# Performance work log

Hardware: AMD Instinct MI355X
Metric: run time of the kernel (lower is better)

## Reference

```python
import jax, jax.numpy as jnp
import numpy as np

DIM = 512; QS = 64; QT = 16; KS = 256; KT = 16; WIN = 4; B = 8; RANK = 32


def build_local_mask():
    # centers = round(linspace(0, kv_steps-1, q_steps)); valid kv step iff |s - center| <= window
    centers = np.round(np.linspace(0.0, KS - 1, QS)).astype(np.int64)
    s = np.arange(KS)
    valid = np.abs(s[None, :] - centers[:, None]) <= WIN  # [QS, KS]
    m = np.where(valid, 0.0, -np.inf).astype(np.float32)
    m = np.repeat(np.repeat(m, QT, axis=0), KT, axis=1)  # [QS*QT, KS*KT]
    return jnp.asarray(m)


def layer_norm(x, g, b, eps=1e-5):
    mu = jnp.mean(x, axis=-1, keepdims=True)
    var = jnp.mean((x - mu) ** 2, axis=-1, keepdims=True)
    return (x - mu) * jax.lax.rsqrt(var + eps) * g + b


def setup_inputs() -> dict:
    key = jax.random.key(0)
    ks = jax.random.split(key, 16)
    w = lambda k, shape: (jax.random.normal(k, shape, jnp.float32) * 0.02)
    return {
        'query': jax.random.normal(ks[0], (B, QS, QT, DIM), jnp.float32),
        'source': jax.random.normal(ks[1], (B, KS, KT, DIM), jnp.float32),
        'ctx0': jax.random.normal(ks[2], (B, DIM), jnp.float32),
        'ctx1': jax.random.normal(ks[3], (B, DIM), jnp.float32),
        'mask': build_local_mask(),
        'qn_g': jnp.ones(DIM), 'qn_b': jnp.zeros(DIM),
        'kvn_g': jnp.ones(DIM), 'kvn_b': jnp.zeros(DIM),
        'Wq': w(ks[4], (DIM, DIM)), 'bq': jnp.zeros(DIM),
        'Wk': w(ks[5], (DIM, DIM)), 'bk': jnp.zeros(DIM),
        'Wv': w(ks[6], (DIM, DIM)), 'bv': jnp.zeros(DIM),
        'Wo': w(ks[7], (DIM, DIM)), 'bo': jnp.zeros(DIM),
        'Wgq': w(ks[8], (DIM, RANK)),
        'Wgk': w(ks[9], (DIM, RANK)),
        'Wc0': w(ks[10], (DIM, DIM)), 'bc0': jnp.zeros(DIM),
        'Wc1': w(ks[11], (DIM, DIM)), 'bc1': jnp.zeros(DIM),
        'Wf': w(ks[12], (DIM, 2 * DIM)), 'bf': jnp.zeros(2 * DIM),
    }


def reference(query, source, ctx0, ctx1, mask, qn_g, qn_b, kvn_g, kvn_b,
              Wq, bq, Wk, bk, Wv, bv, Wo, bo, Wgq, Wgk,
              Wc0, bc0, Wc1, bc1, Wf, bf):
    b = query.shape[0]
    # MultiContextCondition: per-context linear, pooled, FiLM head -> (gamma, beta)
    h = jax.nn.silu(ctx0 @ Wc0 + bc0 + ctx1 @ Wc1 + bc1)          # [b, dim]
    gamma, beta = jnp.split(h @ Wf + bf, 2, axis=-1)              # [b, dim] each
    q_flat = query.reshape(b, QS * QT, DIM)
    s_flat = source.reshape(b, KS * KT, DIM)
    q_base = layer_norm(q_flat, qn_g, qn_b)
    s_base = layer_norm(s_flat, kvn_g, kvn_b)
    q_mod = q_base * (1.0 + gamma[:, None, :]) + beta[:, None, :]
    q_p = q_mod @ Wq + bq
    k_p = s_base @ Wk + bk
    v_p = s_base @ Wv + bv
    scale = DIM ** -0.5
    scores = jnp.einsum('bqd,bkd->bqk', q_p, k_p) * scale          # [b, 1024, 4096]
    gate_q = q_p @ Wgq                                            # [b, q, rank]
    gate_k = k_p @ Wgk                                            # [b, k, rank]
    gate_logits = jnp.einsum('bqr,bkr->bqk', gate_q, gate_k) / np.float32(np.sqrt(RANK))
    gate_bias = jnp.log(jax.nn.sigmoid(gate_logits) + 1e-6)
    scores = scores + mask[None, :, :] + gate_bias
    attn = jax.nn.softmax(scores, axis=-1)
    out = jnp.einsum('bqk,bkd->bqd', attn, v_p) @ Wo + bo
    return out.reshape(b, QS, QT, DIM)
```

## Files before the change

kernel.cpp:

```cpp
#include <hip/hip_runtime.h>
#include <math.h>

#define DIMD 512
#define QS 64
#define KS 256
#define WIN 4
#define BATCH 8
#define RANK 32
#define NQ 1024
#define NK 4096
#define MQ (BATCH*NQ)
#define MK (BATCH*NK)

typedef unsigned short u16;
typedef __attribute__((ext_vector_type(8))) short bf16x8;
typedef __attribute__((ext_vector_type(4))) float f32x4;

__device__ inline u16 f2bf(float x) {
    union { float f; unsigned int u; } v; v.f = x;
    unsigned int r = v.u + 0x7FFF + ((v.u >> 16) & 1);
    return (u16)(r >> 16);
}
__device__ inline float bf2f(u16 x) {
    union { unsigned int u; float f; } v; v.u = ((unsigned int)x) << 16;
    return v.f;
}

__device__ __forceinline__ void gload16(const u16* g, u16* l) {
    __builtin_amdgcn_global_load_lds(
        (const __attribute__((address_space(1))) void*)g,
        (__attribute__((address_space(3))) void*)l, 16, 0, 0);
}


__device__ __forceinline__ void norm0_body(
    int bid, const float* __restrict__ X, const float* __restrict__ g,
    const float* __restrict__ bb, u16* __restrict__ out)
{
    int wave = threadIdx.x >> 6, lane = threadIdx.x & 63;
    long row = (long)bid * 4 + wave;
    const float* x = X + row * DIMD;
    int c = lane * 8;
    float4 a = *(const float4*)&x[c];
    float4 b = *(const float4*)&x[c + 4];
    float s  = a.x + a.y + a.z + a.w + b.x + b.y + b.z + b.w;
    float ss = a.x*a.x + a.y*a.y + a.z*a.z + a.w*a.w
             + b.x*b.x + b.y*b.y + b.z*b.z + b.w*b.w;
    #pragma unroll
    for (int o = 1; o < 64; o <<= 1) { s += __shfl_xor(s, o); ss += __shfl_xor(ss, o); }
    float mu = s * (1.f / DIMD);
    float var = ss * (1.f / DIMD) - mu * mu;
    float rs = rsqrtf(var + 1e-5f);
    float4 g0 = *(const float4*)&g[c],  g1 = *(const float4*)&g[c + 4];
    float4 b0 = *(const float4*)&bb[c], b1 = *(const float4*)&bb[c + 4];
    u16 o8[8];
    o8[0] = f2bf((a.x - mu) * rs * g0.x + b0.x);
    o8[1] = f2bf((a.y - mu) * rs * g0.y + b0.y);
    o8[2] = f2bf((a.z - mu) * rs * g0.z + b0.z);
    o8[3] = f2bf((a.w - mu) * rs * g0.w + b0.w);
    o8[4] = f2bf((b.x - mu) * rs * g1.x + b1.x);
    o8[5] = f2bf((b.y - mu) * rs * g1.y + b1.y);
    o8[6] = f2bf((b.z - mu) * rs * g1.z + b1.z);
    o8[7] = f2bf((b.w - mu) * rs * g1.w + b1.w);
    *(int4*)&out[row * DIMD + c] = *(const int4*)o8;
}

__device__ __forceinline__ void stats_body(
    int bid, const float* __restrict__ X, float* __restrict__ mu_o, float* __restrict__ rs_o)
{
    int wave = threadIdx.x >> 6, lane = threadIdx.x & 63;
    long row = (long)bid * 4 + wave;
    const float* x = X + row * DIMD;
    int c = lane * 8;
    float4 a = *(const float4*)&x[c];
    float4 b = *(const float4*)&x[c + 4];
    float s  = a.x + a.y + a.z + a.w + b.x + b.y + b.z + b.w;
    float ss = a.x*a.x + a.y*a.y + a.z*a.z + a.w*a.w
             + b.x*b.x + b.y*b.y + b.z*b.z + b.w*b.w;
    #pragma unroll
    for (int o = 1; o < 64; o <<= 1) { s += __shfl_xor(s, o); ss += __shfl_xor(ss, o); }
    if (lane == 0) {
        float mu = s * (1.f / DIMD);
        float var = ss * (1.f / DIMD) - mu * mu;
        mu_o[row] = mu;
        rs_o[row] = rsqrtf(var + 1e-5f);
    }
}

__device__ __forceinline__ void film_h_body(
    int bid, const float* __restrict__ ctx0, const float* __restrict__ ctx1,
    const float* __restrict__ Wc0, const float* __restrict__ bc0,
    const float* __restrict__ Wc1, const float* __restrict__ bc1,
    float* __restrict__ h)
{
    int b = bid >> 3;
    int d0 = (bid & 7) * 64;
    int t = threadIdx.x;
    int dl = t >> 2, p = t & 3;
    int d = d0 + dl;
    const float* c0 = ctx0 + b * DIMD;
    const float* c1 = ctx1 + b * DIMD;
    float acc = 0.f;
    #pragma unroll 4
    for (int ii = 0; ii < 128; ii++) {
        int i = p * 128 + ii;
        acc = fmaf(c0[i], Wc0[i * DIMD + d], acc);
        acc = fmaf(c1[i], Wc1[i * DIMD + d], acc);
    }
    acc += __shfl_xor(acc, 1);
    acc += __shfl_xor(acc, 2);
    if (p == 0) {
        float v = acc + bc0[d] + bc1[d];
        h[b * DIMD + d] = v / (1.f + expf(-v));
    }
}

__device__ __forceinline__ void film_gb_body(
    int bid, const float* __restrict__ h, const float* __restrict__ Wf,
    const float* __restrict__ bfv, float* __restrict__ gamma, float* __restrict__ beta)
{
    int b = bid >> 3;
    int d0 = (bid & 7) * 64;
    int t = threadIdx.x;
    int dl = t >> 2, p = t & 3;
    int d = d0 + dl;
    const float* hb = h + b * DIMD;
    float ga = 0.f, be = 0.f;
    #pragma unroll 4
    for (int ii = 0; ii < 128; ii++) {
        int i = p * 128 + ii;
        float hv = hb[i];
        ga = fmaf(hv, Wf[i * 2 * DIMD + d], ga);
        be = fmaf(hv, Wf[i * 2 * DIMD + DIMD + d], be);
    }
    ga += __shfl_xor(ga, 1); ga += __shfl_xor(ga, 2);
    be += __shfl_xor(be, 1); be += __shfl_xor(be, 2);
    if (p == 0) {
        gamma[b * DIMD + d] = ga + bfv[d];
        beta[b * DIMD + d]  = be + bfv[DIMD + d];
    }
}

__device__ __forceinline__ void transpose_body(
    int i, const float* __restrict__ src, u16* __restrict__ dst, int dst_row_off,
    float (*tile)[33])
{
    int t = threadIdx.x;
    int tx = t & 31, ty = t >> 5;
    int bx = (i & 15) * 32;
    int by = (i >> 4) * 32;
    #pragma unroll
    for (int k = 0; k < 4; k++)
        tile[ty + k * 8][tx] = src[(long)(by + ty + k * 8) * DIMD + bx + tx];
    __syncthreads();
    #pragma unroll
    for (int k = 0; k < 4; k++)
        dst[(long)(dst_row_off + bx + ty + k * 8) * DIMD + by + tx] = f2bf(tile[tx][ty + k * 8]);
}

__device__ __forceinline__ void gatefuse_body(
    int idx, const float* __restrict__ W, const float* __restrict__ Wg,
    u16* __restrict__ dst, int dst_row_off)
{
    int r = idx & 31, k = idx >> 5;
    float acc = 0.f;
    #pragma unroll 4
    for (int j = 0; j < DIMD; j++) acc = fmaf(W[k * DIMD + j], Wg[j * RANK + r], acc);
    dst[(long)(dst_row_off + r) * DIMD + k] = f2bf(acc);
}

__device__ __forceinline__ void biascat3_body(
    int bid, const float* __restrict__ b0, const float* __restrict__ b1,
    const float* __restrict__ Wg, float* __restrict__ dst)
{
    int t = bid * 256 + threadIdx.x;
    if (t < 512) dst[t] = b0[t];
    else if (t < 1024) dst[t] = b1[t - 512];
    else if (t < 1056) {
        int r = t - 1024;
        float a = 0.f;
        for (int j = 0; j < DIMD; j++) a = fmaf(b0[j], Wg[j * RANK + r], a);
        dst[t] = a;
    }
}

__device__ __forceinline__ void biascat2_body(
    int bid, const float* __restrict__ b0, const float* __restrict__ Wg,
    float* __restrict__ dst)
{
    int t = bid * 256 + threadIdx.x;
    if (t < 512) dst[t] = b0[t];
    else if (t < 544) {
        int r = t - 512;
        float a = 0.f;
        for (int j = 0; j < DIMD; j++) a = fmaf(b0[j], Wg[j * RANK + r], a);
        dst[t] = a;
    }
}

template<int NSEC, bool BF>
__device__ __forceinline__ void gemm_body(
    int id, const u16* __restrict__ A, const u16* __restrict__ Bt,
    const float* __restrict__ biascat,
    void* __restrict__ C0v, void* __restrict__ C1v, void* __restrict__ Cgv,
    int Nvalid, int nx, int ypg, u16* smem)
{
    u16* As = smem;
    u16* Bs = smem + 4096;

    int t = threadIdx.x;
    int wave = t >> 6, lane = t & 63;
    int xcd = id & 7, li = id >> 3;
    int by = xcd * ypg + li / nx;
    int bx = li % nx;
    int m0 = by * 128, n0 = bx * 128;
    int mhalf = (wave >> 1) * 64, nhalf = (wave & 1) * 64;
    int lm = lane & 15, quad = lane >> 4;

    int srow = wave * 32 + (lane >> 2);
    int scol = (lane & 3) * 8;
    const u16* Ag = A + (long)(m0 + srow) * DIMD + scol;
    const u16* Bg = Bt + (long)(n0 + srow) * DIMD + scol;
    u16* Asl = As + wave * 1024 + lane * 8;
    u16* Bsl = Bs + wave * 1024 + lane * 8;

    f32x4 acc[4][4];
    #pragma unroll
    for (int i = 0; i < 4; i++)
        #pragma unroll
        for (int j = 0; j < 4; j++)
            acc[i][j] = (f32x4){0.f, 0.f, 0.f, 0.f};

    for (int k0 = 0; k0 < DIMD; k0 += 32) {
        __syncthreads();
        gload16(Ag + k0, Asl);
        gload16(Ag + 16 * DIMD + k0, Asl + 512);
        gload16(Bg + k0, Bsl);
        gload16(Bg + 16 * DIMD + k0, Bsl + 512);
        __syncthreads();
        bf16x8 af[4], bfr[4];
        #pragma unroll
        for (int i = 0; i < 4; i++) {
            af[i]  = *(const bf16x8*)&As[(mhalf + i * 16 + lm) * 32 + quad * 8];
            bfr[i] = *(const bf16x8*)&Bs[(nhalf + i * 16 + lm) * 32 + quad * 8];
        }
        #pragma unroll
        for (int i = 0; i < 4; i++)
            #pragma unroll
            for (int j = 0; j < 4; j++)
                acc[i][j] = __builtin_amdgcn_mfma_f32_16x16x32_bf16(af[i], bfr[j], acc[i][j], 0, 0, 0);
    }

    float biasj[4];
    #pragma unroll
    for (int j = 0; j < 4; j++) biasj[j] = biascat[n0 + nhalf + j * 16 + lm];

    if (BF) {
        for (int i = 0; i < 4; i++) {
            __syncthreads();
            #pragma unroll
            for (int j = 0; j < 4; j++)
                #pragma unroll
                for (int r = 0; r < 4; r++)
                    smem[((wave >> 1) * 16 + quad * 4 + r) * 128 + nhalf + j * 16 + lm] =
                        f2bf(acc[i][j][r] + biasj[j]);
            __syncthreads();
            #pragma unroll
            for (int u = 0; u < 2; u++) {
                int cch = t + u * 256;
                int R = cch >> 4, ci = cch & 15;
                long grow = m0 + (R >> 4) * 64 + i * 16 + (R & 15);
                int gcol = n0 + ci * 8;
                int4 val = *(const int4*)&smem[R * 128 + ci * 8];
                if (NSEC == 1) {
                    *(int4*)((u16*)C0v + grow * 512 + gcol) = val;
                } else if (NSEC == 2) {
                    if (gcol < 512)          *(int4*)((u16*)C0v + grow * 512 + gcol) = val;
                    else if (gcol < Nvalid)  *(int4*)((u16*)Cgv + grow * 32 + (gcol - 512)) = val;
                } else {
                    if (gcol < 512)          *(int4*)((u16*)C0v + grow * 512 + gcol) = val;
                    else if (gcol < 1024)    *(int4*)((u16*)C1v + grow * 512 + (gcol - 512)) = val;
                    else if (gcol < Nvalid)  *(int4*)((u16*)Cgv + grow * 32 + (gcol - 1024)) = val;
                }
            }
        }
    } else {
        float* Stg = (float*)smem;
        for (int i = 0; i < 4; i++) {
            __syncthreads();
            #pragma unroll
            for (int j = 0; j < 4; j++)
                #pragma unroll
                for (int r = 0; r < 4; r++)
                    Stg[((wave >> 1) * 16 + quad * 4 + r) * 128 + nhalf + j * 16 + lm] =
                        acc[i][j][r] + biasj[j];
            __syncthreads();
            #pragma unroll
            for (int u = 0; u < 4; u++) {
                int cch = t + u * 256;
                int R = cch >> 5, ci = cch & 31;
                long grow = m0 + (R >> 4) * 64 + i * 16 + (R & 15);
                int gcol = n0 + ci * 4;
                *(float4*)((float*)C0v + grow * 512 + gcol) = *(const float4*)&Stg[R * 128 + ci * 4];
            }
        }
    }
}

#define PREP_NORM0   8192
#define PREP_STATS   (PREP_NORM0 + 2048)
#define PREP_TRANS   (PREP_STATS + 1024)
#define PREP_FILMH   (PREP_TRANS + 64)
#define PREP_GATE    (PREP_FILMH + 128)
#define PREP_TOTAL   (PREP_GATE + 8)

__global__ __launch_bounds__(256) void prep_kernel(
    const float* __restrict__ source, const float* __restrict__ kvn_g,
    const float* __restrict__ kvn_b, u16* __restrict__ sln,
    const float* __restrict__ query, float* __restrict__ mu_q, float* __restrict__ rs_q,
    const float* __restrict__ ctx0, const float* __restrict__ ctx1,
    const float* __restrict__ Wc0, const float* __restrict__ bc0,
    const float* __restrict__ Wc1, const float* __restrict__ bc1,
    float* __restrict__ h,
    const float* __restrict__ Wk, const float* __restrict__ Wv,
    const float* __restrict__ Wq, const float* __restrict__ Wo,
    u16* __restrict__ Btkv, u16* __restrict__ Btq, u16* __restrict__ Bto,
    const float* __restrict__ Wgk, const float* __restrict__ Wgq,
    const float* __restrict__ bk, const float* __restrict__ bv,
    const float* __restrict__ bq, float* __restrict__ biaskv,
    float* __restrict__ biasq)
{
    __shared__ float tile[32][33];
    int bid = blockIdx.x;
    if (bid < PREP_NORM0) {
        norm0_body(bid, source, kvn_g, kvn_b, sln);
    } else if (bid < PREP_STATS) {
        stats_body(bid - PREP_NORM0, query, mu_q, rs_q);
    } else if (bid < PREP_TRANS) {
        int tid = bid - PREP_STATS;
        int which = tid >> 8, i = tid & 255;
        if (which == 0)      transpose_body(i, Wk, Btkv, 0, tile);
        else if (which == 1) transpose_body(i, Wv, Btkv, 512, tile);
        else if (which == 2) transpose_body(i, Wq, Btq, 0, tile);
        else                 transpose_body(i, Wo, Bto, 0, tile);
    } else if (bid < PREP_FILMH) {
        film_h_body(bid - PREP_TRANS, ctx0, ctx1, Wc0, bc0, Wc1, bc1, h);
    } else if (bid < PREP_GATE) {
        int gid = bid - PREP_FILMH;
        int idx = (gid & 63) * 256 + threadIdx.x;
        if (gid < 64) gatefuse_body(idx, Wk, Wgk, Btkv, 1024);
        else          gatefuse_body(idx, Wq, Wgq, Btq, 512);
    } else {
        int cid = bid - PREP_GATE;
        if (cid < 5) biascat3_body(cid, bk, bv, Wgk, biaskv);
        else         biascat2_body(cid - 5, bq, Wgq, biasq);
    }
}

__global__ __launch_bounds__(256) void kv_kernel(
    const float* __restrict__ h, const float* __restrict__ Wf,
    const float* __restrict__ bfv, float* __restrict__ gamma, float* __restrict__ beta,
    const u16* __restrict__ sln, const u16* __restrict__ Btkv,
    const float* __restrict__ biaskv,
    u16* __restrict__ kp, u16* __restrict__ vp, u16* __restrict__ gk)
{
    __shared__ u16 smem[8192];
    int bid = blockIdx.x;
    if (bid < 64) {
        film_gb_body(bid, h, Wf, bfv, gamma, beta);
    } else {
        gemm_body<3, true>(bid - 64, sln, Btkv, biaskv, kp, vp, gk, 1056, 9, 32, smem);
    }
}

__global__ __launch_bounds__(256) void qproj_kernel(
    const float* __restrict__ query, const float* __restrict__ mu_q,
    const float* __restrict__ rs_q, const float* __restrict__ qn_g,
    const float* __restrict__ qn_b, const float* __restrict__ gamma,
    const float* __restrict__ beta, const u16* __restrict__ Btq,
    const float* __restrict__ biasq, u16* __restrict__ qp, u16* __restrict__ gq)
{
    __shared__ u16 smem[8192];
    u16* As = smem;
    u16* Bs = smem + 4096;

    int t = threadIdx.x;
    int wave = t >> 6, lane = t & 63;
    int id = blockIdx.x;
    int xcd = id & 7, li = id >> 3;
    int by = xcd * 8 + li / 5;
    int bx = li % 5;
    int m0 = by * 128, n0 = bx * 128;
    int mhalf = (wave >> 1) * 64, nhalf = (wave & 1) * 64;
    int lm = lane & 15, quad = lane >> 4;
    int bt = m0 >> 10;

    int srow = wave * 32 + (lane >> 2);
    int scol = (lane & 3) * 8;
    const u16* Bg = Btq + (long)(n0 + srow) * DIMD + scol;
    u16* Bsl = Bs + wave * 1024 + lane * 8;

    f32x4 acc[4][4];
    #pragma unroll
    for (int i = 0; i < 4; i++)
        #pragma unroll
        for (int j = 0; j < 4; j++)
            acc[i][j] = (f32x4){0.f, 0.f, 0.f, 0.f};

    for (int k0 = 0; k0 < DIMD; k0 += 32) {
        __syncthreads();
        gload16(Bg + k0, Bsl);
        gload16(Bg + 16 * DIMD + k0, Bsl + 512);
        #pragma unroll
        for (int u = 0; u < 2; u++) {
            int idx = t + u * 256;
            int r = idx >> 2;
            int c8 = (idx & 3) * 8;
            long grow = m0 + r;
            int col = k0 + c8;
            const float* xp = &query[grow * DIMD + col];
            float4 x0 = *(const float4*)xp, x1 = *(const float4*)(xp + 4);
            float mu = mu_q[grow], rs = rs_q[grow];
            float4 g0 = *(const float4*)&qn_g[col], g1 = *(const float4*)&qn_g[col + 4];
            float4 b0 = *(const float4*)&qn_b[col], b1 = *(const float4*)&qn_b[col + 4];
            const float* gp = gamma + bt * DIMD + col;
            const float* bp = beta + bt * DIMD + col;
            float4 gm0 = *(const float4*)gp, gm1 = *(const float4*)(gp + 4);
            float4 be0 = *(const float4*)bp, be1 = *(const float4*)(bp + 4);
            u16 o8[8];
            o8[0] = f2bf(((x0.x - mu) * rs * g0.x + b0.x) * (1.f + gm0.x) + be0.x);
            o8[1] = f2bf(((x0.y - mu) * rs * g0.y + b0.y) * (1.f + gm0.y) + be0.y);
            o8[2] = f2bf(((x0.z - mu) * rs * g0.z + b0.z) * (1.f + gm0.z) + be0.z);
            o8[3] = f2bf(((x0.w - mu) * rs * g0.w + b0.w) * (1.f + gm0.w) + be0.w);
            o8[4] = f2bf(((x1.x - mu) * rs * g1.x + b1.x) * (1.f + gm1.x) + be1.x);
            o8[5] = f2bf(((x1.y - mu) * rs * g1.y + b1.y) * (1.f + gm1.y) + be1.y);
            o8[6] = f2bf(((x1.z - mu) * rs * g1.z + b1.z) * (1.f + gm1.z) + be1.z);
            o8[7] = f2bf(((x1.w - mu) * rs * g1.w + b1.w) * (1.f + gm1.w) + be1.w);
            *(int4*)&As[r * 32 + c8] = *(const int4*)o8;
        }
        __syncthreads();
        bf16x8 af[4], bfr[4];
        #pragma unroll
        for (int i = 0; i < 4; i++) {
            af[i]  = *(const bf16x8*)&As[(mhalf + i * 16 + lm) * 32 + quad * 8];
            bfr[i] = *(const bf16x8*)&Bs[(nhalf + i * 16 + lm) * 32 + quad * 8];
        }
        #pragma unroll
        for (int i = 0; i < 4; i++)
            #pragma unroll
            for (int j = 0; j < 4; j++)
                acc[i][j] = __builtin_amdgcn_mfma_f32_16x16x32_bf16(af[i], bfr[j], acc[i][j], 0, 0, 0);
    }

    float biasj[4];
    #pragma unroll
    for (int j = 0; j < 4; j++) biasj[j] = biasq[n0 + nhalf + j * 16 + lm];

    for (int i = 0; i < 4; i++) {
        __syncthreads();
        #pragma unroll
        for (int j = 0; j < 4; j++)
            #pragma unroll
            for (int r = 0; r < 4; r++)
                smem[((wave >> 1) * 16 + quad * 4 + r) * 128 + nhalf + j * 16 + lm] =
                    f2bf(acc[i][j][r] + biasj[j]);
        __syncthreads();
        #pragma unroll
        for (int u = 0; u < 2; u++) {
            int cch = t + u * 256;
            int R = cch >> 4, ci = cch & 15;
            long grow = m0 + (R >> 4) * 64 + i * 16 + (R & 15);
            int gcol = n0 + ci * 8;
            int4 val = *(const int4*)&smem[R * 128 + ci * 8];
            if (gcol < 512)       *(int4*)(qp + grow * 512 + gcol) = val;
            else if (gcol < 544)  *(int4*)(gq + grow * 32 + (gcol - 512)) = val;
        }
    }
}

__global__ __launch_bounds__(256) void ogemm_kernel(
    const u16* __restrict__ ctxb, const u16* __restrict__ Bto,
    const float* __restrict__ bo, float* __restrict__ out)
{
    __shared__ u16 smem[8192];
    gemm_body<1, false>(blockIdx.x, ctxb, Bto, bo, out, nullptr, nullptr, 512, 4, 8, smem);
}

__global__ __launch_bounds__(256, 2) void attn_kernel(
    const u16* __restrict__ q_bf, const u16* __restrict__ k_bf,
    const u16* __restrict__ v_bf, const u16* __restrict__ gq_bf,
    const u16* __restrict__ gk_bf, u16* __restrict__ ctx)
{
    __shared__ u16 Ks[16 * 512];
    __shared__ u16 Vt[512 * 32];
    __shared__ u16 Pb[16 * 40];
    __shared__ float part[4][16][16];
    __shared__ float Gb[16][16];
    __shared__ float alphap[16];
    __shared__ float linv[16];

    int blk = blockIdx.x;
    int b = blk >> 6, qs = blk & 63;
    int center = (int)(qs * (255.0f / 63.0f) + 0.5f);
    int lo = center - WIN; if (lo < 0) lo = 0;
    int hi = center + WIN; if (hi > KS - 1) hi = KS - 1;
    int nst = hi - lo + 1;
    long rowq0 = (long)b * NQ + qs * 16;
    long rowk0 = (long)b * NK + lo * 16;

    int t = threadIdx.x;
    int wave = t >> 6, lane = t & 63;
    int lm = lane & 15, quad = lane >> 4;
    int qi = t >> 4, ki = t & 15;

    bf16x8 qf[4];
    #pragma unroll
    for (int f = 0; f < 4; f++)
        qf[f] = *(const bf16x8*)&q_bf[(rowq0 + lm) * DIMD + wave * 128 + f * 32 + quad * 8];
    bf16x8 gqf;
    if (wave == 3) gqf = *(const bf16x8*)&gq_bf[(rowq0 + lm) * RANK + quad * 8];

    int4 kpre[4], vpre[4];
    #pragma unroll
    for (int u = 0; u < 4; u++) {
        int idx = u * 256 + t;
        kpre[u] = *(const int4*)&k_bf[(rowk0 + (idx >> 6)) * DIMD + (idx & 63) * 8];
        int vkv = (idx >> 2) & 15, vdc = (idx & 3) | ((idx >> 6) << 2);
        vpre[u] = *(const int4*)&v_bf[(rowk0 + vkv) * DIMD + vdc * 8];
    }

    float m_run = -1e30f, l_run = 0.f;
    f32x4 acc[8];
    #pragma unroll
    for (int j = 0; j < 8; j++) acc[j] = (f32x4){0.f, 0.f, 0.f, 0.f};

    const float scale = 0.044194173824159216f;
    const float grs = 0.17677669529663687f;

    for (int s = 0; s < nst; s++) {
        int half = s & 1;
        #pragma unroll
        for (int u = 0; u < 4; u++) {
            int idx = u * 256 + t;
            int row = idx >> 6, c = idx & 63;
            *(int4*)&Ks[row * 512 + (c ^ (row & 7)) * 8] = kpre[u];
            int vkv = (idx >> 2) & 15, vdc = (idx & 3) | ((idx >> 6) << 2);
            int kvp = half * 16 + vkv;
            u16 vv[8];
            *(int4*)vv = vpre[u];
            #pragma unroll
            for (int i = 0; i < 8; i++) {
                int d = vdc * 8 + i;
                Vt[d * 32 + (((kvp >> 3) ^ (d & 3)) << 3) + (kvp & 7)] = vv[i];
            }
        }
        __syncthreads();
        if (s + 1 < nst) {
            long rk = rowk0 + (long)(s + 1) * 16;
            #pragma unroll
            for (int u = 0; u < 4; u++) {
                int idx = u * 256 + t;
                kpre[u] = *(const int4*)&k_bf[(rk + (idx >> 6)) * DIMD + (idx & 63) * 8];
                int vkv = (idx >> 2) & 15, vdc = (idx & 3) | ((idx >> 6) << 2);
                vpre[u] = *(const int4*)&v_bf[(rk + vkv) * DIMD + vdc * 8];
            }
        }
        f32x4 sacc = (f32x4){0.f, 0.f, 0.f, 0.f};
        #pragma unroll
        for (int f = 0; f < 4; f++) {
            int cidx = wave * 16 + f * 4 + quad;
            bf16x8 kf = *(const bf16x8*)&Ks[lm * 512 + (cidx ^ (lm & 7)) * 8];
            sacc = __builtin_amdgcn_mfma_f32_16x16x32_bf16(qf[f], kf, sacc, 0, 0, 0);
        }
        #pragma unroll
        for (int r = 0; r < 4; r++) part[wave][quad * 4 + r][lm] = sacc[r];
        if (wave == 3) {
            bf16x8 gkf = *(const bf16x8*)&gk_bf[(rowk0 + (long)s * 16 + lm) * RANK + quad * 8];
            f32x4 gacc = (f32x4){0.f, 0.f, 0.f, 0.f};
            gacc = __builtin_amdgcn_mfma_f32_16x16x32_bf16(gqf, gkf, gacc, 0, 0, 0);
            #pragma unroll
            for (int r = 0; r < 4; r++) Gb[quad * 4 + r][lm] = gacc[r];
        }
        __syncthreads();
        float sv = (part[0][qi][ki] + part[1][qi][ki] + part[2][qi][ki] + part[3][qi][ki]) * scale;
        float gl = Gb[qi][ki] * grs;
        float sig = 1.f / (1.f + expf(-gl));
        sv += logf(sig + 1e-6f);
        float mx = sv;
        mx = fmaxf(mx, __shfl_xor(mx, 1));
        mx = fmaxf(mx, __shfl_xor(mx, 2));
        mx = fmaxf(mx, __shfl_xor(mx, 4));
        mx = fmaxf(mx, __shfl_xor(mx, 8));
        float m_new = fmaxf(m_run, mx);
        float p = expf(sv - m_new);
        float ps = p;
        ps += __shfl_xor(ps, 1);
        ps += __shfl_xor(ps, 2);
        ps += __shfl_xor(ps, 4);
        ps += __shfl_xor(ps, 8);
        float alpha = expf(m_run - m_new);
        l_run = l_run * alpha + ps;
        m_run = m_new;
        Pb[qi * 40 + half * 16 + ki] = f2bf(p);
        if (half == 1) {
            Pb[qi * 40 + ki] = f2bf(bf2f(Pb[qi * 40 + ki]) * alpha);
        }
        bool dopv = (half == 1) || (s == nst - 1);
        if (dopv && half == 0) Pb[qi * 40 + 16 + ki] = 0;
        if (ki == 0) {
            if (half == 0) alphap[qi] = alpha;
            else           alphap[qi] *= alpha;
            if (s == nst - 1) linv[qi] = 1.f / l_run;
        }
        __syncthreads();
        if (dopv) {
            float ar[4];
            #pragma unroll
            for (int r = 0; r < 4; r++) ar[r] = alphap[quad * 4 + r];
            #pragma unroll
            for (int j = 0; j < 8; j++)
                #pragma unroll
                for (int r = 0; r < 4; r++) acc[j][r] *= ar[r];
            bf16x8 pf = *(const bf16x8*)&Pb[lm * 40 + quad * 8];
            #pragma unroll
            for (int j = 0; j < 8; j++) {
                int d = wave * 128 + j * 16 + lm;
                bf16x8 vf = *(const bf16x8*)&Vt[d * 32 + ((quad ^ (d & 3)) << 3)];
                acc[j] = __builtin_amdgcn_mfma_f32_16x16x32_bf16(pf, vf, acc[j], 0, 0, 0);
            }
            __syncthreads();
        }
    }
    float li[4];
    #pragma unroll
    for (int r = 0; r < 4; r++) li[r] = linv[quad * 4 + r];
    #pragma unroll
    for (int j = 0; j < 8; j++) {
        int d = wave * 128 + j * 16 + lm;
        #pragma unroll
        for (int r = 0; r < 4; r++)
            ctx[(rowq0 + quad * 4 + r) * DIMD + d] = f2bf(acc[j][r] * li[r]);
    }
}

extern "C" void kernel_launch(void* const* d_in, const int* in_sizes, int n_in,
                              void* d_out, int out_size, void* d_ws, size_t ws_size,
                              hipStream_t stream) {
    const float* query  = (const float*)d_in[0];
    const float* source = (const float*)d_in[1];
    const float* ctx0   = (const float*)d_in[2];
    const float* ctx1   = (const float*)d_in[3];
    const float* qn_g  = (const float*)d_in[5];
    const float* qn_b  = (const float*)d_in[6];
    const float* kvn_g = (const float*)d_in[7];
    const float* kvn_b = (const float*)d_in[8];
    const float* Wq = (const float*)d_in[9];   const float* bq = (const float*)d_in[10];
    const float* Wk = (const float*)d_in[11];  const float* bk = (const float*)d_in[12];
    const float* Wv = (const float*)d_in[13];  const float* bv = (const float*)d_in[14];
    const float* Wo = (const float*)d_in[15];  const float* bo = (const float*)d_in[16];
    const float* Wgq = (const float*)d_in[17];
    const float* Wgk = (const float*)d_in[18];
    const float* Wc0 = (const float*)d_in[19]; const float* bc0 = (const float*)d_in[20];
    const float* Wc1 = (const float*)d_in[21]; const float* bc1 = (const float*)d_in[22];
    const float* Wf  = (const float*)d_in[23]; const float* bfv = (const float*)d_in[24];

    float* ws = (float*)d_ws;
    float* h      = ws;
    float* gamma  = h + 4096;
    float* beta   = gamma + 4096;
    float* biaskv = beta + 4096;
    float* biasq  = biaskv + 1152;
    float* mu_q   = biasq + 640;
    float* rs_q   = mu_q + 8192;
    u16* u = (u16*)(rs_q + 8192);
    u16* sln  = u;                 u += (long)MK * DIMD;
    u16* kp   = u;                 u += (long)MK * DIMD;
    u16* vp   = u;                 u += (long)MK * DIMD;
    u16* gk   = u;                 u += (long)MK * RANK;
    u16* gq   = u;                 u += (long)MQ * RANK;
    u16* qp   = u;                 u += (long)MQ * DIMD;
    u16* ctxb = u;                 u += (long)MQ * DIMD;
    u16* Btkv = u;                 u += 1152L * DIMD;
    u16* Btq  = u;                 u += 640L * DIMD;
    u16* Bto  = u;                 u += 512L * DIMD;
    float* out = (float*)d_out;

    prep_kernel<<<PREP_TOTAL, 256, 0, stream>>>(
        source, kvn_g, kvn_b, sln,
        query, mu_q, rs_q,
        ctx0, ctx1, Wc0, bc0, Wc1, bc1, h,
        Wk, Wv, Wq, Wo, Btkv, Btq, Bto,
        Wgk, Wgq, bk, bv, bq, biaskv, biasq);

    kv_kernel<<<64 + 2304, 256, 0, stream>>>(
        h, Wf, bfv, gamma, beta, sln, Btkv, biaskv, kp, vp, gk);

    qproj_kernel<<<320, 256, 0, stream>>>(
        query, mu_q, rs_q, qn_g, qn_b, gamma, beta, Btq, biasq, qp, gq);

    attn_kernel<<<BATCH * QS, 256, 0, stream>>>(qp, kp, vp, gq, gk, ctxb);

    ogemm_kernel<<<256, 256, 0, stream>>>(ctxb, Bto, bo, out);
}
```

Measured before the change: 354.8 us.

## Fuse all stages into one persistent-dependency mega kernel with atomic flags

Replaces the five separate launches with a single kernel whose block ranges handle each stage. Inter-stage ordering now comes from per-tile atomic counters that consumer blocks spin on, so later stages can start as soon as their inputs are ready instead of waiting at kernel boundaries. It also merges the two FiLM steps into one block per batch, stages Wg in LDS for the gate-fused weights, and processes four rows per wave in the norm and stats stages. The scheme relies on blocks being dispatched in index order to avoid deadlock. Spin-waiting and the larger 64KB shared allocation may lower occupancy for the GEMM and attention stages.

```diff
diff --git a/kernel.cpp b/kernel.cpp
--- a/kernel.cpp
+++ b/kernel.cpp
@@ -32,117 +32,81 @@
         (__attribute__((address_space(3))) void*)l, 16, 0, 0);
 }
 
-
-__device__ __forceinline__ void norm0_body(
-    int bid, const float* __restrict__ X, const float* __restrict__ g,
-    const float* __restrict__ bb, u16* __restrict__ out)
-{
-    int wave = threadIdx.x >> 6, lane = threadIdx.x & 63;
-    long row = (long)bid * 4 + wave;
-    const float* x = X + row * DIMD;
-    int c = lane * 8;
-    float4 a = *(const float4*)&x[c];
-    float4 b = *(const float4*)&x[c + 4];
-    float s  = a.x + a.y + a.z + a.w + b.x + b.y + b.z + b.w;
-    float ss = a.x*a.x + a.y*a.y + a.z*a.z + a.w*a.w
-             + b.x*b.x + b.y*b.y + b.z*b.z + b.w*b.w;
-    #pragma unroll
-    for (int o = 1; o < 64; o <<= 1) { s += __shfl_xor(s, o); ss += __shfl_xor(ss, o); }
-    float mu = s * (1.f / DIMD);
-    float var = ss * (1.f / DIMD) - mu * mu;
-    float rs = rsqrtf(var + 1e-5f);
-    float4 g0 = *(const float4*)&g[c],  g1 = *(const float4*)&g[c + 4];
-    float4 b0 = *(const float4*)&bb[c], b1 = *(const float4*)&bb[c + 4];
-    u16 o8[8];
-    o8[0] = f2bf((a.x - mu) * rs * g0.x + b0.x);
-    o8[1] = f2bf((a.y - mu) * rs * g0.y + b0.y);
-    o8[2] = f2bf((a.z - mu) * rs * g0.z + b0.z);
-    o8[3] = f2bf((a.w - mu) * rs * g0.w + b0.w);
-    o8[4] = f2bf((b.x - mu) * rs * g1.x + b1.x);
-    o8[5] = f2bf((b.y - mu) * rs * g1.y + b1.y);
-    o8[6] = f2bf((b.z - mu) * rs * g1.z + b1.z);
-    o8[7] = f2bf((b.w - mu) * rs * g1.w + b1.w);
-    *(int4*)&out[row * DIMD + c] = *(const int4*)o8;
-}
-
-__device__ __forceinline__ void stats_body(
-    int bid, const float* __restrict__ X, float* __restrict__ mu_o, float* __restrict__ rs_o)
-{
-    int wave = threadIdx.x >> 6, lane = threadIdx.x & 63;
-    long row = (long)bid * 4 + wave;
-    const float* x = X + row * DIMD;
-    int c = lane * 8;
-    float4 a = *(const float4*)&x[c];
-    float4 b = *(const float4*)&x[c + 4];
-    float s  = a.x + a.y + a.z + a.w + b.x + b.y + b.z + b.w;
-    float ss = a.x*a.x + a.y*a.y + a.z*a.z + a.w*a.w
-             + b.x*b.x + b.y*b.y + b.z*b.z + b.w*b.w;
-    #pragma unroll
-    for (int o = 1; o < 64; o <<= 1) { s += __shfl_xor(s, o); ss += __shfl_xor(ss, o); }
-    if (lane == 0) {
-        float mu = s * (1.f / DIMD);
-        float var = ss * (1.f / DIMD) - mu * mu;
-        mu_o[row] = mu;
-        rs_o[row] = rsqrtf(var + 1e-5f);
-    }
-}
-
-__device__ __forceinline__ void film_h_body(
-    int bid, const float* __restrict__ ctx0, const float* __restrict__ ctx1,
+__device__ __forceinline__ void sigflag(int* f) {
+    __hip_atomic_fetch_add(f, 1, __ATOMIC_RELEASE, __HIP_MEMORY_SCOPE_AGENT);
+}
+__device__ __forceinline__ void waitflag(int* f, int target) {
+    if (threadIdx.x == 0) {
+        for (int i = 0; i < (1 << 22); i++) {
+            if (__hip_atomic_load(f, __ATOMIC_RELAXED, __HIP_MEMORY_SCOPE_AGENT) >= target)
+                break;
+            __builtin_amdgcn_s_sleep(8);
+        }
+    }
+    __syncthreads();
+}
+
+
+__device__ __forceinline__ void film_body(
+    int b, const float* __restrict__ ctx0, const float* __restrict__ ctx1,
     const float* __restrict__ Wc0, const float* __restrict__ bc0,
     const float* __restrict__ Wc1, const float* __restrict__ bc1,
-    float* __restrict__ h)
-{
-    int b = bid >> 3;
-    int d0 = (bid & 7) * 64;
+    const float* __restrict__ Wf, const float* __restrict__ bfv,
+    float* __restrict__ gamma, float* __restrict__ beta, float* hL)
+{
     int t = threadIdx.x;
-    int dl = t >> 2, p = t & 3;
-    int d = d0 + dl;
     const float* c0 = ctx0 + b * DIMD;
     const float* c1 = ctx1 + b * DIMD;
+    #pragma unroll
+    for (int half = 0; half < 2; half++) {
+        int d = t + half * 256;
+        float acc = bc0[d] + bc1[d];
+        #pragma unroll 4
+        for (int i = 0; i < DIMD; i++)
+            acc = fmaf(c0[i], Wc0[i * DIMD + d], fmaf(c1[i], Wc1[i * DIMD + d], acc));
+        hL[d] = acc / (1.f + expf(-acc));
+    }
+    __syncthreads();
+    #pragma unroll
+    for (int half = 0; half < 2; half++) {
+        int d = t + half * 256;
+        float ga = 0.f, be = 0.f;
+        #pragma unroll 4
+        for (int i = 0; i < DIMD; i++) {
+            float hv = hL[i];
+            ga = fmaf(hv, Wf[i * 2 * DIMD + d], ga);
+            be = fmaf(hv, Wf[i * 2 * DIMD + DIMD + d], be);
+        }
+        gamma[b * DIMD + d] = ga + bfv[d];
+        beta[b * DIMD + d]  = be + bfv[DIMD + d];
+    }
+}
+
+__device__ __forceinline__ void gatefuse_body(
+    int gid, const float* __restrict__ W, const float* __restrict__ Wg,
+    u16* __restrict__ dst, int off, float* WgL)
+{
+    int t = threadIdx.x;
+    for (int i = t; i < 4096; i += 256)
+        ((float4*)WgL)[i] = ((const float4*)Wg)[i];
+    __syncthreads();
+    int idx = gid * 256 + t;
+    int r = idx & 31, k = idx >> 5;
+    const float* Wr = W + (long)k * DIMD;
     float acc = 0.f;
     #pragma unroll 4
-    for (int ii = 0; ii < 128; ii++) {
-        int i = p * 128 + ii;
-        acc = fmaf(c0[i], Wc0[i * DIMD + d], acc);
-        acc = fmaf(c1[i], Wc1[i * DIMD + d], acc);
-    }
-    acc += __shfl_xor(acc, 1);
-    acc += __shfl_xor(acc, 2);
-    if (p == 0) {
-        float v = acc + bc0[d] + bc1[d];
-        h[b * DIMD + d] = v / (1.f + expf(-v));
-    }
-}
-
-__device__ __forceinline__ void film_gb_body(
-    int bid, const float* __restrict__ h, const float* __restrict__ Wf,
-    const float* __restrict__ bfv, float* __restrict__ gamma, float* __restrict__ beta)
-{
-    int b = bid >> 3;
-    int d0 = (bid & 7) * 64;
-    int t = threadIdx.x;
-    int dl = t >> 2, p = t & 3;
-    int d = d0 + dl;
-    const float* hb = h + b * DIMD;
-    float ga = 0.f, be = 0.f;
-    #pragma unroll 4
-    for (int ii = 0; ii < 128; ii++) {
-        int i = p * 128 + ii;
-        float hv = hb[i];
-        ga = fmaf(hv, Wf[i * 2 * DIMD + d], ga);
-        be = fmaf(hv, Wf[i * 2 * DIMD + DIMD + d], be);
-    }
-    ga += __shfl_xor(ga, 1); ga += __shfl_xor(ga, 2);
-    be += __shfl_xor(be, 1); be += __shfl_xor(be, 2);
-    if (p == 0) {
-        gamma[b * DIMD + d] = ga + bfv[d];
-        beta[b * DIMD + d]  = be + bfv[DIMD + d];
-    }
+    for (int j = 0; j < DIMD; j += 4) {
+        float4 w4 = *(const float4*)&Wr[j];
+        acc = fmaf(w4.x, WgL[(j + 0) * 32 + r], acc);
+        acc = fmaf(w4.y, WgL[(j + 1) * 32 + r], acc);
+        acc = fmaf(w4.z, WgL[(j + 2) * 32 + r], acc);
+        acc = fmaf(w4.w, WgL[(j + 3) * 32 + r], acc);
+    }
+    dst[(long)(off + r) * DIMD + k] = f2bf(acc);
 }
 
 __device__ __forceinline__ void transpose_body(
-    int i, const float* __restrict__ src, u16* __restrict__ dst, int dst_row_off,
+    int i, const float* __restrict__ src, u16* __restrict__ dst, int off,
     float (*tile)[33])
 {
     int t = threadIdx.x;
@@ -155,18 +119,7 @@
     __syncthreads();
     #pragma unroll
     for (int k = 0; k < 4; k++)
-        dst[(long)(dst_row_off + bx + ty + k * 8) * DIMD + by + tx] = f2bf(tile[tx][ty + k * 8]);
-}
-
-__device__ __forceinline__ void gatefuse_body(
-    int idx, const float* __restrict__ W, const float* __restrict__ Wg,
-    u16* __restrict__ dst, int dst_row_off)
-{
-    int r = idx & 31, k = idx >> 5;
-    float acc = 0.f;
-    #pragma unroll 4
-    for (int j = 0; j < DIMD; j++) acc = fmaf(W[k * DIMD + j], Wg[j * RANK + r], acc);
-    dst[(long)(dst_row_off + r) * DIMD + k] = f2bf(acc);
+        dst[(long)(off + bx + ty + k * 8) * DIMD + by + tx] = f2bf(tile[tx][ty + k * 8]);
 }
 
 __device__ __forceinline__ void biascat3_body(
@@ -183,7 +136,6 @@
         dst[t] = a;
     }
 }
-
 __device__ __forceinline__ void biascat2_body(
     int bid, const float* __restrict__ b0, const float* __restrict__ Wg,
     float* __restrict__ dst)
@@ -198,22 +150,79 @@
     }
 }
 
+__device__ __forceinline__ void norm0_body(
+    int bid, const float* __restrict__ X, const float* __restrict__ g,
+    const float* __restrict__ bb, u16* __restrict__ out)
+{
+    int wave = threadIdx.x >> 6, lane = threadIdx.x & 63;
+    int c = lane * 8;
+    float4 g0 = *(const float4*)&g[c],  g1 = *(const float4*)&g[c + 4];
+    float4 b0 = *(const float4*)&bb[c], b1 = *(const float4*)&bb[c + 4];
+    long row0 = (long)bid * 16 + wave * 4;
+    #pragma unroll
+    for (int rr = 0; rr < 4; rr++) {
+        long row = row0 + rr;
+        const float* x = X + row * DIMD;
+        float4 a = *(const float4*)&x[c];
+        float4 b = *(const float4*)&x[c + 4];
+        float s  = a.x + a.y + a.z + a.w + b.x + b.y + b.z + b.w;
+        float ss = a.x*a.x + a.y*a.y + a.z*a.z + a.w*a.w
+                 + b.x*b.x + b.y*b.y + b.z*b.z + b.w*b.w;
+        #pragma unroll
+        for (int o = 1; o < 64; o <<= 1) { s += __shfl_xor(s, o); ss += __shfl_xor(ss, o); }
+        float mu = s * (1.f / DIMD);
+        float var = ss * (1.f / DIMD) - mu * mu;
+        float rs = rsqrtf(var + 1e-5f);
+        u16 o8[8];
+        o8[0] = f2bf((a.x - mu) * rs * g0.x + b0.x);
+        o8[1] = f2bf((a.y - mu) * rs * g0.y + b0.y);
+        o8[2] = f2bf((a.z - mu) * rs * g0.z + b0.z);
+        o8[3] = f2bf((a.w - mu) * rs * g0.w + b0.w);
+        o8[4] = f2bf((b.x - mu) * rs * g1.x + b1.x);
+        o8[5] = f2bf((b.y - mu) * rs * g1.y + b1.y);
+        o8[6] = f2bf((b.z - mu) * rs * g1.z + b1.z);
+        o8[7] = f2bf((b.w - mu) * rs * g1.w + b1.w);
+        *(int4*)&out[row * DIMD + c] = *(const int4*)o8;
+    }
+}
+
+__device__ __forceinline__ void stats_body(
+    int bid, const float* __restrict__ X, float* __restrict__ mu_o, float* __restrict__ rs_o)
+{
+    int wave = threadIdx.x >> 6, lane = threadIdx.x & 63;
+    int c = lane * 8;
+    long row0 = (long)bid * 16 + wave * 4;
+    #pragma unroll
+    for (int rr = 0; rr < 4; rr++) {
+        long row = row0 + rr;
+        const float* x = X + row * DIMD;
+        float4 a = *(const float4*)&x[c];
+        float4 b = *(const float4*)&x[c + 4];
+        float s  = a.x + a.y + a.z + a.w + b.x + b.y + b.z + b.w;
+        float ss = a.x*a.x + a.y*a.y + a.z*a.z + a.w*a.w
+                 + b.x*b.x + b.y*b.y + b.z*b.z + b.w*b.w;
+        #pragma unroll
+        for (int o = 1; o < 64; o <<= 1) { s += __shfl_xor(s, o); ss += __shfl_xor(ss, o); }
+        if (lane == 0) {
+            float mu = s * (1.f / DIMD);
+            float var = ss * (1.f / DIMD) - mu * mu;
+            mu_o[row] = mu;
+            rs_o[row] = rsqrtf(var + 1e-5f);
+        }
+    }
+}
+
 template<int NSEC, bool BF>
 __device__ __forceinline__ void gemm_body(
-    int id, const u16* __restrict__ A, const u16* __restrict__ Bt,
+    int m0, int n0, const u16* __restrict__ A, const u16* __restrict__ Bt,
     const float* __restrict__ biascat,
     void* __restrict__ C0v, void* __restrict__ C1v, void* __restrict__ Cgv,
-    int Nvalid, int nx, int ypg, u16* smem)
+    int Nvalid, u16* smem)
 {
     u16* As = smem;
     u16* Bs = smem + 4096;
-
     int t = threadIdx.x;
     int wave = t >> 6, lane = t & 63;
-    int xcd = id & 7, li = id >> 3;
-    int by = xcd * ypg + li / nx;
-    int bx = li % nx;
-    int m0 = by * 128, n0 = bx * 128;
     int mhalf = (wave >> 1) * 64, nhalf = (wave & 1) * 64;
     int lm = lane & 15, quad = lane >> 4;
 
@@ -307,90 +316,18 @@
     }
 }
 
-#define PREP_NORM0   8192
-#define PREP_STATS   (PREP_NORM0 + 2048)
-#define PREP_TRANS   (PREP_STATS + 1024)
-#define PREP_FILMH   (PREP_TRANS + 64)
-#define PREP_GATE    (PREP_FILMH + 128)
-#define PREP_TOTAL   (PREP_GATE + 8)
-
-__global__ __launch_bounds__(256) void prep_kernel(
-    const float* __restrict__ source, const float* __restrict__ kvn_g,
-    const float* __restrict__ kvn_b, u16* __restrict__ sln,
-    const float* __restrict__ query, float* __restrict__ mu_q, float* __restrict__ rs_q,
-    const float* __restrict__ ctx0, const float* __restrict__ ctx1,
-    const float* __restrict__ Wc0, const float* __restrict__ bc0,
-    const float* __restrict__ Wc1, const float* __restrict__ bc1,
-    float* __restrict__ h,
-    const float* __restrict__ Wk, const float* __restrict__ Wv,
-    const float* __restrict__ Wq, const float* __restrict__ Wo,
-    u16* __restrict__ Btkv, u16* __restrict__ Btq, u16* __restrict__ Bto,
-    const float* __restrict__ Wgk, const float* __restrict__ Wgq,
-    const float* __restrict__ bk, const float* __restrict__ bv,
-    const float* __restrict__ bq, float* __restrict__ biaskv,
-    float* __restrict__ biasq)
-{
-    __shared__ float tile[32][33];
-    int bid = blockIdx.x;
-    if (bid < PREP_NORM0) {
-        norm0_body(bid, source, kvn_g, kvn_b, sln);
-    } else if (bid < PREP_STATS) {
-        stats_body(bid - PREP_NORM0, query, mu_q, rs_q);
-    } else if (bid < PREP_TRANS) {
-        int tid = bid - PREP_STATS;
-        int which = tid >> 8, i = tid & 255;
-        if (which == 0)      transpose_body(i, Wk, Btkv, 0, tile);
-        else if (which == 1) transpose_body(i, Wv, Btkv, 512, tile);
-        else if (which == 2) transpose_body(i, Wq, Btq, 0, tile);
-        else                 transpose_body(i, Wo, Bto, 0, tile);
-    } else if (bid < PREP_FILMH) {
-        film_h_body(bid - PREP_TRANS, ctx0, ctx1, Wc0, bc0, Wc1, bc1, h);
-    } else if (bid < PREP_GATE) {
-        int gid = bid - PREP_FILMH;
-        int idx = (gid & 63) * 256 + threadIdx.x;
-        if (gid < 64) gatefuse_body(idx, Wk, Wgk, Btkv, 1024);
-        else          gatefuse_body(idx, Wq, Wgq, Btq, 512);
-    } else {
-        int cid = bid - PREP_GATE;
-        if (cid < 5) biascat3_body(cid, bk, bv, Wgk, biaskv);
-        else         biascat2_body(cid - 5, bq, Wgq, biasq);
-    }
-}
-
-__global__ __launch_bounds__(256) void kv_kernel(
-    const float* __restrict__ h, const float* __restrict__ Wf,
-    const float* __restrict__ bfv, float* __restrict__ gamma, float* __restrict__ beta,
-    const u16* __restrict__ sln, const u16* __restrict__ Btkv,
-    const float* __restrict__ biaskv,
-    u16* __restrict__ kp, u16* __restrict__ vp, u16* __restrict__ gk)
-{
-    __shared__ u16 smem[8192];
-    int bid = blockIdx.x;
-    if (bid < 64) {
-        film_gb_body(bid, h, Wf, bfv, gamma, beta);
-    } else {
-        gemm_body<3, true>(bid - 64, sln, Btkv, biaskv, kp, vp, gk, 1056, 9, 32, smem);
-    }
-}
-
-__global__ __launch_bounds__(256) void qproj_kernel(
-    const float* __restrict__ query, const float* __restrict__ mu_q,
+__device__ __forceinline__ void qproj_body(
+    int m0, int n0, const float* __restrict__ query, const float* __restrict__ mu_q,
     const float* __restrict__ rs_q, const float* __restrict__ qn_g,
     const float* __restrict__ qn_b, const float* __restrict__ gamma,
     const float* __restrict__ beta, const u16* __restrict__ Btq,
-    const float* __restrict__ biasq, u16* __restrict__ qp, u16* __restrict__ gq)
-{
-    __shared__ u16 smem[8192];
+    const float* __restrict__ biasq, u16* __restrict__ qp, u16* __restrict__ gq,
+    u16* smem)
+{
     u16* As = smem;
     u16* Bs = smem + 4096;
-
     int t = threadIdx.x;
     int wave = t >> 6, lane = t & 63;
-    int id = blockIdx.x;
-    int xcd = id & 7, li = id >> 3;
-    int by = xcd * 8 + li / 5;
-    int bx = li % 5;
-    int m0 = by * 128, n0 = bx * 128;
     int mhalf = (wave >> 1) * 64, nhalf = (wave & 1) * 64;
     int lm = lane & 15, quad = lane >> 4;
     int bt = m0 >> 10;
@@ -478,28 +415,19 @@
     }
 }
 
-__global__ __launch_bounds__(256) void ogemm_kernel(
-    const u16* __restrict__ ctxb, const u16* __restrict__ Bto,
-    const float* __restrict__ bo, float* __restrict__ out)
-{
-    __shared__ u16 smem[8192];
-    gemm_body<1, false>(blockIdx.x, ctxb, Bto, bo, out, nullptr, nullptr, 512, 4, 8, smem);
-}
-
-__global__ __launch_bounds__(256, 2) void attn_kernel(
-    const u16* __restrict__ q_bf, const u16* __restrict__ k_bf,
+__device__ __forceinline__ void attn_body(
+    int blk, const u16* __restrict__ q_bf, const u16* __restrict__ k_bf,
     const u16* __restrict__ v_bf, const u16* __restrict__ gq_bf,
-    const u16* __restrict__ gk_bf, u16* __restrict__ ctx)
-{
-    __shared__ u16 Ks[16 * 512];
-    __shared__ u16 Vt[512 * 32];
-    __shared__ u16 Pb[16 * 40];
-    __shared__ float part[4][16][16];
-    __shared__ float Gb[16][16];
-    __shared__ float alphap[16];
-    __shared__ float linv[16];
-
-    int blk = blockIdx.x;
+    const u16* __restrict__ gk_bf, u16* __restrict__ ctx, char* SM)
+{
+    u16* Ks = (u16*)SM;
+    u16* Vt = (u16*)(SM + 16384);
+    u16* Pb = (u16*)(SM + 49152);
+    float* part = (float*)(SM + 50432);
+    float* Gb = (float*)(SM + 54528);
+    float* alphap = (float*)(SM + 55552);
+    float* linv = (float*)(SM + 55616);
+
     int b = blk >> 6, qs = blk & 63;
     int center = (int)(qs * (255.0f / 63.0f) + 0.5f);
     int lo = center - WIN; if (lo < 0) lo = 0;
@@ -573,17 +501,18 @@
             sacc = __builtin_amdgcn_mfma_f32_16x16x32_bf16(qf[f], kf, sacc, 0, 0, 0);
         }
         #pragma unroll
-        for (int r = 0; r < 4; r++) part[wave][quad * 4 + r][lm] = sacc[r];
+        for (int r = 0; r < 4; r++) part[wave * 256 + (quad * 4 + r) * 16 + lm] = sacc[r];
         if (wave == 3) {
             bf16x8 gkf = *(const bf16x8*)&gk_bf[(rowk0 + (long)s * 16 + lm) * RANK + quad * 8];
             f32x4 gacc = (f32x4){0.f, 0.f, 0.f, 0.f};
             gacc = __builtin_amdgcn_mfma_f32_16x16x32_bf16(gqf, gkf, gacc, 0, 0, 0);
             #pragma unroll
-            for (int r = 0; r < 4; r++) Gb[quad * 4 + r][lm] = gacc[r];
-        }
-        __syncthreads();
-        float sv = (part[0][qi][ki] + part[1][qi][ki] + part[2][qi][ki] + part[3][qi][ki]) * scale;
-        float gl = Gb[qi][ki] * grs;
+            for (int r = 0; r < 4; r++) Gb[(quad * 4 + r) * 16 + lm] = gacc[r];
+        }
+        __syncthreads();
+        float sv = (part[qi * 16 + ki] + part[256 + qi * 16 + ki]
+                  + part[512 + qi * 16 + ki] + part[768 + qi * 16 + ki]) * scale;
+        float gl = Gb[qi * 16 + ki] * grs;
         float sig = 1.f / (1.f + expf(-gl));
         sv += logf(sig + 1e-6f);
         float mx = sv;
@@ -643,6 +572,141 @@
     }
 }
 
+#define B_FILM  0
+#define B_GATE  8
+#define B_TRANS 136
+#define B_BIAS  1160
+#define B_STAT  1168
+#define B_NORM  1680
+#define B_KV    3728
+#define B_QP    6032
+#define B_ATTN  6352
+#define B_OG    6864
+#define B_TOTAL 7120
+
+__global__ __launch_bounds__(256, 2) void mega_kernel(
+    int* __restrict__ F,
+    const float* __restrict__ query, const float* __restrict__ source,
+    const float* __restrict__ ctx0, const float* __restrict__ ctx1,
+    const float* __restrict__ qn_g, const float* __restrict__ qn_b,
+    const float* __restrict__ kvn_g, const float* __restrict__ kvn_b,
+    const float* __restrict__ Wq, const float* __restrict__ bq,
+    const float* __restrict__ Wk, const float* __restrict__ bk,
+    const float* __restrict__ Wv, const float* __restrict__ bv,
+    const float* __restrict__ Wo, const float* __restrict__ bo,
+    const float* __restrict__ Wgq, const float* __restrict__ Wgk,
+    const float* __restrict__ Wc0, const float* __restrict__ bc0,
+    const float* __restrict__ Wc1, const float* __restrict__ bc1,
+    const float* __restrict__ Wf, const float* __restrict__ bfv,
+    float* __restrict__ gamma, float* __restrict__ beta,
+    float* __restrict__ biaskv, float* __restrict__ biasq,
+    float* __restrict__ mu_q, float* __restrict__ rs_q,
+    u16* __restrict__ sln, u16* __restrict__ kp, u16* __restrict__ vp,
+    u16* __restrict__ gk, u16* __restrict__ gq, u16* __restrict__ qp,
+    u16* __restrict__ ctxb, u16* __restrict__ Btkv, u16* __restrict__ Btq,
+    u16* __restrict__ Bto, float* __restrict__ out)
+{
+    __shared__ __align__(16) char SM[65536];
+    int* F_SLN = F;
+    int* F_QST = F + 256;
+    int* F_FILM = F + 320;
+    int* F_WKV = F + 321;
+    int* F_WQ  = F + 322;
+    int* F_WO  = F + 323;
+    int* F_KV  = F + 324;
+    int* F_QP  = F + 580;
+    int* F_CTX = F + 644;
+
+    int bid = blockIdx.x;
+
+    if (bid < B_GATE) {
+        film_body(bid, ctx0, ctx1, Wc0, bc0, Wc1, bc1, Wf, bfv, gamma, beta, (float*)SM);
+        __syncthreads();
+        if (threadIdx.x == 0) sigflag(F_FILM);
+    } else if (bid < B_TRANS) {
+        int gid = bid - B_GATE;
+        if (gid < 64) {
+            gatefuse_body(gid, Wk, Wgk, Btkv, 1024, (float*)SM);
+            __syncthreads();
+            if (threadIdx.x == 0) sigflag(F_WKV);
+        } else {
+            gatefuse_body(gid - 64, Wq, Wgq, Btq, 512, (float*)SM);
+            __syncthreads();
+            if (threadIdx.x == 0) sigflag(F_WQ);
+        }
+    } else if (bid < B_BIAS) {
+        int tid = bid - B_TRANS;
+        int which = tid >> 8, i = tid & 255;
+        float (*tile)[33] = (float(*)[33])SM;
+        if (which == 0)      { transpose_body(i, Wk, Btkv, 0, tile);   __syncthreads(); if (threadIdx.x == 0) sigflag(F_WKV); }
+        else if (which == 1) { transpose_body(i, Wv, Btkv, 512, tile); __syncthreads(); if (threadIdx.x == 0) sigflag(F_WKV); }
+        else if (which == 2) { transpose_body(i, Wq, Btq, 0, tile);    __syncthreads(); if (threadIdx.x == 0) sigflag(F_WQ); }
+        else                 { transpose_body(i, Wo, Bto, 0, tile);    __syncthreads(); if (threadIdx.x == 0) sigflag(F_WO); }
+    } else if (bid < B_STAT) {
+        int cid = bid - B_BIAS;
+        if (cid < 5) { biascat3_body(cid, bk, bv, Wgk, biaskv); __syncthreads(); if (threadIdx.x == 0) sigflag(F_WKV); }
+        else         { biascat2_body(cid - 5, bq, Wgq, biasq);  __syncthreads(); if (threadIdx.x == 0) sigflag(F_WQ); }
+    } else if (bid < B_NORM) {
+        int sid = bid - B_STAT;
+        stats_body(sid, query, mu_q, rs_q);
+        __syncthreads();
+        if (threadIdx.x == 0) sigflag(&F_QST[sid >> 3]);
+    } else if (bid < B_KV) {
+        int nid = bid - B_NORM;
+        norm0_body(nid, source, kvn_g, kvn_b, sln);
+        __syncthreads();
+        if (threadIdx.x == 0) sigflag(&F_SLN[nid >> 3]);
+    } else if (bid < B_QP) {
+        int l = bid - B_KV;
+        int xcd = l & 7, li = l >> 3;
+        int by = xcd * 32 + li / 9;
+        int bx = li % 9;
+        waitflag(F_WKV, 581);
+        waitflag(&F_SLN[by], 8);
+        gemm_body<3, true>(by * 128, bx * 128, sln, Btkv, biaskv, kp, vp, gk, 1056, (u16*)SM);
+        __syncthreads();
+        if (threadIdx.x == 0) sigflag(&F_KV[by]);
+    } else if (bid < B_ATTN) {
+        int l = bid - B_QP;
+        int xcd = l & 7, li = l >> 3;
+        int by = xcd * 8 + li / 5;
+        int bx = li % 5;
+        waitflag(F_WQ, 323);
+        waitflag(F_FILM, 8);
+        waitflag(&F_QST[by], 8);
+        qproj_body(by * 128, bx * 128, query, mu_q, rs_q, qn_g, qn_b, gamma, beta,
+                   Btq, biasq, qp, gq, (u16*)SM);
+        __syncthreads();
+        if (threadIdx.x == 0) sigflag(&F_QP[by]);
+    } else if (bid < B_OG) {
+        int blk = bid - B_ATTN;
+        int b = blk >> 6, qs = blk & 63;
+        int center = (int)(qs * (255.0f / 63.0f) + 0.5f);
+        int lo = center - WIN; if (lo < 0) lo = 0;
+        int hi = center + WIN; if (hi > KS - 1) hi = KS - 1;
+        int nst = hi - lo + 1;
+        int rowk0 = b * NK + lo * 16;
+        int gby0 = rowk0 >> 7;
+        int gby1 = (rowk0 + nst * 16 - 1) >> 7;
+        int qg = (b * NQ + qs * 16) >> 7;
+        waitflag(&F_QP[qg], 5);
+        waitflag(&F_KV[gby0], 9);
+        if (gby1 != gby0) waitflag(&F_KV[gby1], 9);
+        attn_body(blk, qp, kp, vp, gq, gk, ctxb, SM);
+        __syncthreads();
+        if (threadIdx.x == 0) sigflag(&F_CTX[b * 8 + (qs >> 3)]);
+    } else {
+        int l = bid - B_OG;
+        int xcd = l & 7, li = l >> 3;
+        int by = xcd * 8 + li / 4;
+        int bx = li % 4;
+        waitflag(F_WO, 256);
+        waitflag(&F_CTX[by], 8);
+        gemm_body<1, false>(by * 128, bx * 128, ctxb, Bto, bo, out, nullptr, nullptr,
+                            512, (u16*)SM);
+    }
+}
+
 extern "C" void kernel_launch(void* const* d_in, const int* in_sizes, int n_in,
                               void* d_out, int out_size, void* d_ws, size_t ws_size,
                               hipStream_t stream) {
@@ -664,9 +728,9 @@
     const float* Wc1 = (const float*)d_in[21]; const float* bc1 = (const float*)d_in[22];
     const float* Wf  = (const float*)d_in[23]; const float* bfv = (const float*)d_in[24];
 
-    float* ws = (float*)d_ws;
-    float* h      = ws;
-    float* gamma  = h + 4096;
+    int* flags = (int*)d_ws;
+    float* fbase  = (float*)((char*)d_ws + 4096);
+    float* gamma  = fbase;
     float* beta   = gamma + 4096;
     float* biaskv = beta + 4096;
     float* biasq  = biaskv + 1152;
@@ -685,20 +749,13 @@
     u16* Bto  = u;                 u += 512L * DIMD;
     float* out = (float*)d_out;
 
-    prep_kernel<<<PREP_TOTAL, 256, 0, stream>>>(
-        source, kvn_g, kvn_b, sln,
-        query, mu_q, rs_q,
-        ctx0, ctx1, Wc0, bc0, Wc1, bc1, h,
-        Wk, Wv, Wq, Wo, Btkv, Btq, Bto,
-        Wgk, Wgq, bk, bv, bq, biaskv, biasq);
-
-    kv_kernel<<<64 + 2304, 256, 0, stream>>>(
-        h, Wf, bfv, gamma, beta, sln, Btkv, biaskv, kp, vp, gk);
-
-    qproj_kernel<<<320, 256, 0, stream>>>(
-        query, mu_q, rs_q, qn_g, qn_b, gamma, beta, Btq, biasq, qp, gq);
-
-    attn_kernel<<<BATCH * QS, 256, 0, stream>>>(qp, kp, vp, gq, gk, ctxb);
-
-    ogemm_kernel<<<256, 256, 0, stream>>>(ctxb, Bto, bo, out);
-}
+    hipMemsetAsync(d_ws, 0, 4096, stream);
+
+    mega_kernel<<<B_TOTAL, 256, 0, stream>>>(
+        flags,
+        query, source, ctx0, ctx1, qn_g, qn_b, kvn_g, kvn_b,
+        Wq, bq, Wk, bk, Wv, bv, Wo, bo, Wgq, Wgk,
+        Wc0, bc0, Wc1, bc1, Wf, bfv,
+        gamma, beta, biaskv, biasq, mu_q, rs_q,
+        sln, kp, vp, gk, gq, qp, ctxb, Btkv, Btq, Bto, out);
+}
```

New measurement: 706.7 us. 99.2% more time.
